# Optimization experiments

Hardware: AMD Instinct MI355X
Metric: run time of the kernel (lower is better)

## Reference

```python
import jax, jax.numpy as jnp
import numpy as np

EPS = 1e-06


def setup_inputs() -> dict:
    key = jax.random.key(0)
    k1, k2 = jax.random.split(key)
    N, C, H, W = 256, 3, 256, 256
    preds = jax.random.normal(k1, (N, C, H, W), dtype=jnp.float32)
    targets = jax.random.normal(k2, (N, C, H, W), dtype=jnp.float32)
    return {"preds": preds, "targets": targets}


def reference(preds, targets):
    N = preds.shape[0]
    # Flatten to [N, D] as in torch's .view(len, -1)
    Z = targets.reshape(N, -1)  # targets first, matching the torch call order
    B = preds.reshape(N, -1)
    Z_c = Z - jnp.mean(Z, axis=1, keepdims=True)
    B_c = B - jnp.mean(B, axis=1, keepdims=True)
    # Full N x N cross-correlation matrix (faithful to original), then diagonal
    num = jnp.einsum('nd,md->nm', Z_c, B_c)
    Z_norm = jnp.linalg.norm(Z_c, axis=1, keepdims=True)  # [N,1]
    B_norm = jnp.linalg.norm(B_c, axis=1, keepdims=True)  # [N,1]
    denom = Z_norm @ B_norm.T  # [N,N]
    pearson = num / (denom + EPS)
    corr = jnp.diagonal(pearson)  # [N]
    return jnp.mean(corr)  # reduction='mean'
```

## Files before the change

kernel.cpp:

```cpp
#include <hip/hip_runtime.h>


constexpr int NROWS = 256;
constexpr int D     = 3 * 256 * 256;
constexpr int D4    = D / 4;
constexpr int TPB   = 1024;
constexpr double EPS = 1e-6;

__global__ __launch_bounds__(TPB) void row_corr_kernel(
        const float4* __restrict__ preds,
        const float4* __restrict__ targets,
        double* __restrict__ row_out)
{
    const int  row  = blockIdx.x;
    const int  tid  = threadIdx.x;
    const long base = (long)row * D4;

    double sZ = 0.0, sB = 0.0, sZZ = 0.0, sBB = 0.0, sZB = 0.0;

    for (int i = tid; i < D4; i += TPB) {
        const float4 b4 = preds[base + i];
        const float4 z4 = targets[base + i];
        double z, b;
        z = (double)z4.x; b = (double)b4.x;
        sZ += z; sB += b; sZZ = fma(z, z, sZZ); sBB = fma(b, b, sBB); sZB = fma(z, b, sZB);
        z = (double)z4.y; b = (double)b4.y;
        sZ += z; sB += b; sZZ = fma(z, z, sZZ); sBB = fma(b, b, sBB); sZB = fma(z, b, sZB);
        z = (double)z4.z; b = (double)b4.z;
        sZ += z; sB += b; sZZ = fma(z, z, sZZ); sBB = fma(b, b, sBB); sZB = fma(z, b, sZB);
        z = (double)z4.w; b = (double)b4.w;
        sZ += z; sB += b; sZZ = fma(z, z, sZZ); sBB = fma(b, b, sBB); sZB = fma(z, b, sZB);
    }

    #pragma unroll
    for (int off = 32; off > 0; off >>= 1) {
        sZ  += __shfl_down(sZ,  off);
        sB  += __shfl_down(sB,  off);
        sZZ += __shfl_down(sZZ, off);
        sBB += __shfl_down(sBB, off);
        sZB += __shfl_down(sZB, off);
    }

    constexpr int NWAVES = TPB / 64;
    __shared__ double sm[5][NWAVES];
    const int wave = tid >> 6;
    const int lane = tid & 63;
    if (lane == 0) {
        sm[0][wave] = sZ;  sm[1][wave] = sB;
        sm[2][wave] = sZZ; sm[3][wave] = sBB;
        sm[4][wave] = sZB;
    }
    __syncthreads();

    if (tid == 0) {
        double tZ = 0, tB = 0, tZZ = 0, tBB = 0, tZB = 0;
        #pragma unroll
        for (int w = 0; w < NWAVES; ++w) {
            tZ += sm[0][w]; tB += sm[1][w]; tZZ += sm[2][w];
            tBB += sm[3][w]; tZB += sm[4][w];
        }
        const double invD = 1.0 / (double)D;
        const double num  = tZB - tZ * tB * invD;
        const double varZ = fmax(tZZ - tZ * tZ * invD, 0.0);
        const double varB = fmax(tBB - tB * tB * invD, 0.0);
        const double den  = sqrt(varZ) * sqrt(varB) + EPS;
        row_out[row] = num / den;
    }
}

__global__ __launch_bounds__(NROWS) void mean_kernel(
        const double* __restrict__ row_out, float* __restrict__ out)
{
    const int tid = threadIdx.x;
    double v = row_out[tid];
    #pragma unroll
    for (int off = 32; off > 0; off >>= 1) v += __shfl_down(v, off);

    __shared__ double sm[NROWS / 64];
    const int wave = tid >> 6;
    const int lane = tid & 63;
    if (lane == 0) sm[wave] = v;
    __syncthreads();
    if (tid == 0) {
        double t = 0.0;
        #pragma unroll
        for (int w = 0; w < NROWS / 64; ++w) t += sm[w];
        out[0] = (float)(t / (double)NROWS);
    }
}

extern "C" void kernel_launch(void* const* d_in, const int* in_sizes, int n_in,
                              void* d_out, int out_size, void* d_ws, size_t ws_size,
                              hipStream_t stream) {
    const float4* preds   = (const float4*)d_in[0];
    const float4* targets = (const float4*)d_in[1];
    double* row_out = (double*)d_ws;
    float*  out     = (float*)d_out;

    hipLaunchKernelGGL(row_corr_kernel, dim3(NROWS), dim3(TPB), 0, stream,
                       preds, targets, row_out);
    hipLaunchKernelGGL(mean_kernel, dim3(1), dim3(NROWS), 0, stream,
                       row_out, out);
}
```

Measured before the change: 390.3 us.

## Split each row across 16 blocks and unroll loads for more memory parallelism

Each row's reduction now runs in 16 chunk blocks of 256 threads instead of one 1024-thread block per row. That gives 4096 blocks rather than 256, so the work spreads more evenly over the CUs. Each thread issues four float4 loads from each input before doing the FP64 accumulations, which keeps more memory requests in flight. Per-chunk sums go to the workspace, and the finish kernel combines them per row before taking the mean, at the cost of a small extra workspace traffic pass.

Result: no change. 393.7 us (+0.9%).

```diff
diff --git a/kernel.cpp b/kernel.cpp
--- a/kernel.cpp
+++ b/kernel.cpp
@@ -1,35 +1,49 @@
 #include <hip/hip_runtime.h>
 
 
-constexpr int NROWS = 256;
-constexpr int D     = 3 * 256 * 256;
-constexpr int D4    = D / 4;
-constexpr int TPB   = 1024;
+constexpr int NROWS  = 256;
+constexpr int D      = 3 * 256 * 256;
+constexpr int D4     = D / 4;
+constexpr int CHUNKS = 16;
+constexpr int TPB1   = 256;
+constexpr int C4     = D4 / CHUNKS;
+constexpr int ITERS  = C4 / TPB1;
 constexpr double EPS = 1e-6;
 
-__global__ __launch_bounds__(TPB) void row_corr_kernel(
+__global__ __launch_bounds__(TPB1) void partial_kernel(
         const float4* __restrict__ preds,
         const float4* __restrict__ targets,
-        double* __restrict__ row_out)
+        double* __restrict__ partials)
 {
-    const int  row  = blockIdx.x;
-    const int  tid  = threadIdx.x;
-    const long base = (long)row * D4;
+    const int  blk   = blockIdx.x;
+    const int  row   = blk / CHUNKS;
+    const int  chunk = blk % CHUNKS;
+    const int  tid   = threadIdx.x;
+    const long base  = (long)row * D4 + (long)chunk * C4 + tid;
 
     double sZ = 0.0, sB = 0.0, sZZ = 0.0, sBB = 0.0, sZB = 0.0;
 
-    for (int i = tid; i < D4; i += TPB) {
-        const float4 b4 = preds[base + i];
-        const float4 z4 = targets[base + i];
-        double z, b;
-        z = (double)z4.x; b = (double)b4.x;
-        sZ += z; sB += b; sZZ = fma(z, z, sZZ); sBB = fma(b, b, sBB); sZB = fma(z, b, sZB);
-        z = (double)z4.y; b = (double)b4.y;
-        sZ += z; sB += b; sZZ = fma(z, z, sZZ); sBB = fma(b, b, sBB); sZB = fma(z, b, sZB);
-        z = (double)z4.z; b = (double)b4.z;
-        sZ += z; sB += b; sZZ = fma(z, z, sZZ); sBB = fma(b, b, sBB); sZB = fma(z, b, sZB);
-        z = (double)z4.w; b = (double)b4.w;
-        sZ += z; sB += b; sZZ = fma(z, z, sZZ); sBB = fma(b, b, sBB); sZB = fma(z, b, sZB);
+    #pragma unroll
+    for (int it = 0; it < ITERS; it += 4) {
+        float4 z4[4], b4[4];
+        #pragma unroll
+        for (int u = 0; u < 4; ++u) {
+            const long idx = base + (long)(it + u) * TPB1;
+            b4[u] = preds[idx];
+            z4[u] = targets[idx];
+        }
+        #pragma unroll
+        for (int u = 0; u < 4; ++u) {
+            double z, b;
+            z = (double)z4[u].x; b = (double)b4[u].x;
+            sZ += z; sB += b; sZZ = fma(z,z,sZZ); sBB = fma(b,b,sBB); sZB = fma(z,b,sZB);
+            z = (double)z4[u].y; b = (double)b4[u].y;
+            sZ += z; sB += b; sZZ = fma(z,z,sZZ); sBB = fma(b,b,sBB); sZB = fma(z,b,sZB);
+            z = (double)z4[u].z; b = (double)b4[u].z;
+            sZ += z; sB += b; sZZ = fma(z,z,sZZ); sBB = fma(b,b,sBB); sZB = fma(z,b,sZB);
+            z = (double)z4[u].w; b = (double)b4[u].w;
+            sZ += z; sB += b; sZZ = fma(z,z,sZZ); sBB = fma(b,b,sBB); sZB = fma(z,b,sZB);
+        }
     }
 
     #pragma unroll
@@ -41,7 +55,7 @@
         sZB += __shfl_down(sZB, off);
     }
 
-    constexpr int NWAVES = TPB / 64;
+    constexpr int NWAVES = TPB1 / 64;
     __shared__ double sm[5][NWAVES];
     const int wave = tid >> 6;
     const int lane = tid & 63;
@@ -53,35 +67,50 @@
     __syncthreads();
 
     if (tid == 0) {
-        double tZ = 0, tB = 0, tZZ = 0, tBB = 0, tZB = 0;
+        double t[5];
         #pragma unroll
-        for (int w = 0; w < NWAVES; ++w) {
-            tZ += sm[0][w]; tB += sm[1][w]; tZZ += sm[2][w];
-            tBB += sm[3][w]; tZB += sm[4][w];
+        for (int k = 0; k < 5; ++k) {
+            double acc = 0.0;
+            #pragma unroll
+            for (int w = 0; w < NWAVES; ++w) acc += sm[k][w];
+            t[k] = acc;
         }
-        const double invD = 1.0 / (double)D;
-        const double num  = tZB - tZ * tB * invD;
-        const double varZ = fmax(tZZ - tZ * tZ * invD, 0.0);
-        const double varB = fmax(tBB - tB * tB * invD, 0.0);
-        const double den  = sqrt(varZ) * sqrt(varB) + EPS;
-        row_out[row] = num / den;
+        double* out = partials + (long)blk * 5;
+        #pragma unroll
+        for (int k = 0; k < 5; ++k) out[k] = t[k];
     }
 }
 
-__global__ __launch_bounds__(NROWS) void mean_kernel(
-        const double* __restrict__ row_out, float* __restrict__ out)
+__global__ __launch_bounds__(NROWS) void finish_kernel(
+        const double* __restrict__ partials, float* __restrict__ out)
 {
-    const int tid = threadIdx.x;
-    double v = row_out[tid];
+    const int r = threadIdx.x;
+    double tZ = 0, tB = 0, tZZ = 0, tBB = 0, tZB = 0;
+    const double* p = partials + (long)r * CHUNKS * 5;
+    #pragma unroll
+    for (int c = 0; c < CHUNKS; ++c) {
+        tZ  += p[c * 5 + 0];
+        tB  += p[c * 5 + 1];
+        tZZ += p[c * 5 + 2];
+        tBB += p[c * 5 + 3];
+        tZB += p[c * 5 + 4];
+    }
+    const double invD = 1.0 / (double)D;
+    const double num  = tZB - tZ * tB * invD;
+    const double varZ = fmax(tZZ - tZ * tZ * invD, 0.0);
+    const double varB = fmax(tBB - tB * tB * invD, 0.0);
+    const double den  = sqrt(varZ) * sqrt(varB) + EPS;
+    double v = num / den;
+
     #pragma unroll
     for (int off = 32; off > 0; off >>= 1) v += __shfl_down(v, off);
 
     __shared__ double sm[NROWS / 64];
-    const int wave = tid >> 6;
-    const int lane = tid & 63;
+    const int wave = r >> 6;
+    const int lane = r & 63;
     if (lane == 0) sm[wave] = v;
     __syncthreads();
-    if (tid == 0) {
+    if (r == 0) {
         double t = 0.0;
         #pragma unroll
         for (int w = 0; w < NROWS / 64; ++w) t += sm[w];
@@ -94,11 +123,11 @@
                               hipStream_t stream) {
     const float4* preds   = (const float4*)d_in[0];
     const float4* targets = (const float4*)d_in[1];
-    double* row_out = (double*)d_ws;
-    float*  out     = (float*)d_out;
+    double* partials = (double*)d_ws;
+    float*  out      = (float*)d_out;
 
-    hipLaunchKernelGGL(row_corr_kernel, dim3(NROWS), dim3(TPB), 0, stream,
-                       preds, targets, row_out);
-    hipLaunchKernelGGL(mean_kernel, dim3(1), dim3(NROWS), 0, stream,
-                       row_out, out);
+    hipLaunchKernelGGL(partial_kernel, dim3(NROWS * CHUNKS), dim3(TPB1), 0, stream,
+                       preds, targets, partials);
+    hipLaunchKernelGGL(finish_kernel, dim3(1), dim3(NROWS), 0, stream,
+                       partials, out);
 }
```
